# Kernel tuning notes

Hardware: AMD Instinct MI355X
Metric: run time of the kernel (lower is better)

## Reference

```python
import jax, jax.numpy as jnp
import numpy as np

EPS = 1.1920929e-07  # torch.finfo(torch.float32).eps
R = 2
K = 2 * R - 1  # 3x3 directional kernels

# kornia normalized sobel kernels (divided by sum of |k| = 8)
_SOBEL_X = np.array([[-1.0, 0.0, 1.0], [-2.0, 0.0, 2.0], [-1.0, 0.0, 1.0]], np.float32) / 8.0
_SOBEL_Y = _SOBEL_X.T.copy()


def _conv2d_same(x, k2d, pad_mode):
    """Depthwise 'same' cross-correlation of x:[B,C,H,W] with a single [kh,kw] kernel."""
    B, C, H, W = x.shape
    kh, kw = k2d.shape
    ph, pw = kh // 2, kw // 2
    xp = jnp.pad(x, ((0, 0), (0, 0), (ph, ph), (pw, pw)), mode=pad_mode)
    xr = xp.reshape(B * C, 1, H + 2 * ph, W + 2 * pw)
    kr = jnp.asarray(k2d, x.dtype)[None, None]  # [1,1,kh,kw]
    y = jax.lax.conv_general_dilated(
        xr, kr, window_strides=(1, 1), padding='VALID',
        dimension_numbers=('NCHW', 'OIHW', 'NCHW'))
    return y.reshape(B, C, H, W)


def _spatial_gradient(x):
    # kornia SpatialGradient(mode='sobel', normalized=True) with replicate padding
    gx = _conv2d_same(x, _SOBEL_X, 'edge')
    gy = _conv2d_same(x, _SOBEL_Y, 'edge')
    return gx, gy


def _edge_theta(true_labels):
    gx, gy = _spatial_gradient(true_labels)
    gxx, _ = _spatial_gradient(gx)       # second_grad_x[:, :, 0]
    gxy, gyy = _spatial_gradient(gy)     # second_grad_y[:, :, 0], [:, :, 1]
    theta = jnp.fmod(
        jnp.arctan(gyy * jnp.sign(-gxy + EPS) / (gxx + EPS)),
        np.float32(np.pi))
    return theta


def _directional_kernels():
    vert = np.zeros((K, K), np.float32); vert[:, R - 1] = 1.0   # ones column
    horiz = np.zeros((K, K), np.float32); horiz[R - 1, :] = 1.0  # ones row
    lead = np.eye(K, dtype=np.float32)
    cnt = np.fliplr(np.eye(K, dtype=np.float32)).copy()
    return horiz, vert, lead, cnt


def setup_inputs() -> dict:
    key = jax.random.key(0)
    k1, k2 = jax.random.split(key)
    true_labels = jax.random.uniform(k1, (8, 2, 1024, 1024), dtype=jnp.float32)
    pred_labels = jax.random.normal(k2, (8, 2, 1024, 1024), dtype=jnp.float32)
    return {"true_labels": true_labels, "pred_labels": pred_labels}


def reference(true_labels, pred_labels):
    theta = _edge_theta(true_labels)
    # quantize edge direction into 5 bins
    thresh_theta = jnp.fmod(jnp.round(theta * (5.0 / np.float32(np.pi))) + 5.0, 5.0)
    exp_preds = jnp.exp(pred_labels)

    horiz_k, vert_k, lead_k, cnt_k = _directional_kernels()
    # kornia filter2D default: reflect padding, no normalization
    horiz_f = _conv2d_same(exp_preds, horiz_k, 'reflect')
    vert_f = _conv2d_same(exp_preds, vert_k, 'reflect')
    lead_f = _conv2d_same(exp_preds, lead_k, 'reflect')
    cnt_f = _conv2d_same(exp_preds, cnt_k, 'reflect')

    horiz_nms = (thresh_theta == 0).astype(exp_preds.dtype) * (exp_preds / (horiz_f + EPS))
    vert_nms = (thresh_theta == 2).astype(exp_preds.dtype) * (exp_preds / (vert_f + EPS))
    lead_nms = (thresh_theta == 3).astype(exp_preds.dtype) * (exp_preds / (lead_f + EPS))
    cnt_nms = (thresh_theta == 1).astype(exp_preds.dtype) * (exp_preds / (cnt_f + EPS))

    # cat along new dim then total sum == sum of the four partial sums
    nms_loss = horiz_nms.sum() + vert_nms.sum() + lead_nms.sum() + cnt_nms.sum()
    return nms_loss
```

## Files before the change

### kernel.cpp

```cpp
#include <hip/hip_runtime.h>

#define HHI 1024
#define WWI 1024
#define NI  16
#define EPSF  1.1920929e-07f
#define EPS64 7.62939453125e-06f
#define T1 0.3249196962329063f
#define T2 1.3763819204711735f

#define GX  16
#define GYB 8
#define FRB 4
#define NB_INT (GX * GYB * NI)
#define NB_FRM (FRB * GYB * NI)
#define NB_TOT (NB_INT + NB_FRM)
#define NFRAME 8176

__device__ __forceinline__ int clampi(int v, int hi) { return v < 0 ? 0 : (v > hi ? hi : v); }
__device__ __forceinline__ int refli(int v, int n)  { return v < 0 ? -v : (v >= n ? 2*n-2-v : v); }
__device__ __forceinline__ float frcp(float x) { return __builtin_amdgcn_rcpf(x); }

template <bool USE_WS>
__global__ __launch_bounds__(256, 6) void nms_main(
    const float* __restrict__ tru, const float* __restrict__ prd,
    float* __restrict__ partial)
{
    __shared__ float sred[4];
    const int tid  = threadIdx.x;
    const int lane = tid & 63;
    const int wave = tid >> 6;
    const int z = blockIdx.z;
    const float* timg = tru + (size_t)z * (HHI * WWI);
    const float* pimg = prd + (size_t)z * (HHI * WWI);
    float term = 0.f;

    if (blockIdx.x < GX) {
        const int x  = blockIdx.x * 64 + lane;
        const int Y0 = blockIdx.y * 128 + wave * 32;
        const int ci0 = clampi(x - 2, WWI - 1);
        const int ci1 = clampi(x - 1, WWI - 1);
        const int ci2 = x;
        const int ci3 = clampi(x + 1, WWI - 1);
        const int ci4 = clampi(x + 2, WWI - 1);
        const bool mx = (x >= 2) & (x <= WWI - 3);
        float H1[5], H2[5], H3[5];
        #pragma unroll 1
        for (int ch = 0; ch < 8; ++ch) {
            #pragma unroll
            for (int pos = 0; pos < 5; ++pos) {
                const int i = ch * 5 + pos;
                if (i < 36) {
                    const int s  = Y0 - 2 + i;
                    const int gy = clampi(s, HHI - 1);
                    const float* trow = timg + (size_t)gy * WWI;
                    float t0 = trow[ci0], t1 = trow[ci1], t2 = trow[ci2],
                          t3 = trow[ci3], t4 = trow[ci4];
                    float s04 = t0 + t4, s13 = t1 + t3;
                    H1[pos] = s04 - 2.f * t2;
                    H2[pos] = s04 + 4.f * s13 + 6.f * t2;
                    H3[pos] = (t4 - t0) + 2.f * (t3 - t1);
                    if (i >= 4) {
                        const int y = s - 2;
                        if (y >= 2 && y <= HHI - 3) {
                            const int q0 = (pos + 1) % 5, q1 = (pos + 2) % 5,
                                      q2 = (pos + 3) % 5, q3 = (pos + 4) % 5, q4 = pos;
                            float gxx = (H1[q0] + H1[q4]) + 4.f * (H1[q1] + H1[q3]) + 6.f * H1[q2];
                            float gyy = (H2[q0] + H2[q4]) - 2.f * H2[q2];
                            float gxy = (H3[q4] - H3[q0]) + 2.f * (H3[q3] - H3[q1]);
                            float sarg = EPS64 - gxy;
                            float num = (sarg > 0.f) ? gyy : ((sarg < 0.f) ? -gyy : 0.f);
                            float v = num * frcp(gxx + EPS64);
                            bool c2v = (v > T2);
                            bool c1v = (v > T1) & !c2v;
                            bool c0v = (v >= -T1) & (v <= T1);
                            bool c3v = (v < -T2);
                            bool have = c2v | c1v | c0v | c3v;
                            int dr  = c0v ? 0 : 1;
                            int co1 = c2v ? ci2 : (c1v ? ci3 : ci1);
                            int co2 = c2v ? ci2 : (c1v ? ci1 : ci3);
                            float ec = __expf(pimg[(size_t)y * WWI + ci2]);
                            float d1 = __expf(pimg[(size_t)(y - dr) * WWI + co1]);
                            float d2 = __expf(pimg[(size_t)(y + dr) * WWI + co2]);
                            float val = ec * frcp(d1 + ec + d2 + EPSF);
                            term += (have & mx) ? val : 0.f;
                        }
                    }
                }
            }
        }
    } else {
        const int fid = (blockIdx.x - GX) * GYB + blockIdx.y;
        const int p = fid * 256 + tid;
        const bool valid = p < NFRAME;
        int y, x;
        if (p < 2048)      { y = p >> 10;                x = p & 1023; }
        else if (p < 4096) { y = 1022 + ((p - 2048) >> 10); x = p & 1023; }
        else { int q = p - 4096; y = 2 + (q >> 2); int xi = q & 3; x = (xi < 2) ? xi : 1020 + xi; }
        if (!valid) { y = 2; x = 0; }

        int R1[3], C1[3], R2[3][3], C2[3][3];
        #pragma unroll
        for (int a = 0; a < 3; ++a) { R1[a] = clampi(y + a - 1, HHI - 1); C1[a] = clampi(x + a - 1, WWI - 1); }
        #pragma unroll
        for (int a = 0; a < 3; ++a)
            #pragma unroll
            for (int e = 0; e < 3; ++e) {
                R2[a][e] = clampi(R1[a] + e - 1, HHI - 1);
                C2[a][e] = clampi(C1[a] + e - 1, WWI - 1);
            }
        const int hx[3] = {-1, 0, 1}, vx[3] = {1, 2, 1};
        const int hy[3] = {1, 2, 1},  vy[3] = {-1, 0, 1};
        float gxu[3][3], gyu[3][3];
        #pragma unroll
        for (int a = 0; a < 3; ++a)
            #pragma unroll
            for (int b = 0; b < 3; ++b) {
                float sx = 0.f, sy = 0.f;
                #pragma unroll
                for (int e = 0; e < 3; ++e)
                    #pragma unroll
                    for (int f = 0; f < 3; ++f) {
                        const int wx = hx[f] * vx[e], wy = hy[f] * vy[e];
                        if (wx | wy) {
                            float tv = timg[(size_t)R2[a][e] * WWI + C2[b][f]];
                            if (wx) sx += (float)wx * tv;
                            if (wy) sy += (float)wy * tv;
                        }
                    }
                gxu[a][b] = sx; gyu[a][b] = sy;
            }
        float gxx = 0.f, gxy = 0.f, gyy = 0.f;
        #pragma unroll
        for (int a = 0; a < 3; ++a)
            #pragma unroll
            for (int b = 0; b < 3; ++b) {
                const int w1 = hx[b] * vx[a], w2 = hy[b] * vy[a];
                if (w1) { gxx += (float)w1 * gxu[a][b]; gxy += (float)w1 * gyu[a][b]; }
                if (w2) { gyy += (float)w2 * gyu[a][b]; }
            }
        float sarg = EPS64 - gxy;
        float num = (sarg > 0.f) ? gyy : ((sarg < 0.f) ? -gyy : 0.f);
        float v = num * frcp(gxx + EPS64);
        bool c2v = (v > T2);
        bool c1v = (v > T1) & !c2v;
        bool c0v = (v >= -T1) & (v <= T1);
        bool c3v = (v < -T2);
        bool have = c2v | c1v | c0v | c3v;
        int r1 = c0v ? y : refli(y - 1, HHI);
        int r2 = c0v ? y : refli(y + 1, HHI);
        int xm = refli(x - 1, WWI), xp = refli(x + 1, WWI);
        int co1 = c2v ? x : (c1v ? xp : xm);
        int co2 = c2v ? x : (c1v ? xm : xp);
        float ec = __expf(pimg[(size_t)y * WWI + x]);
        float d1 = __expf(pimg[(size_t)r1 * WWI + co1]);
        float d2 = __expf(pimg[(size_t)r2 * WWI + co2]);
        float val = ec * frcp(d1 + ec + d2 + EPSF);
        term += (have & valid) ? val : 0.f;
    }

    for (int off = 32; off; off >>= 1) term += __shfl_down(term, off, 64);
    if (lane == 0) sred[wave] = term;
    __syncthreads();
    if (tid == 0) {
        float b = sred[0] + sred[1] + sred[2] + sred[3];
        if (USE_WS) {
            const int slot = (blockIdx.x < GX)
                ? ((z * GYB + blockIdx.y) * GX + blockIdx.x)
                : (NB_INT + z * 32 + ((blockIdx.x - GX) * GYB + blockIdx.y));
            partial[slot] = b;
        } else {
            atomicAdd(partial, b);
        }
    }
}

__global__ __launch_bounds__(1024) void reduce_kernel(
    const float* __restrict__ partial, float* __restrict__ out)
{
    __shared__ float s_red[16];
    float s = 0.f;
    for (int i = threadIdx.x; i < NB_TOT; i += 1024) s += partial[i];
    for (int off = 32; off; off >>= 1) s += __shfl_down(s, off, 64);
    if ((threadIdx.x & 63) == 0) s_red[threadIdx.x >> 6] = s;
    __syncthreads();
    if (threadIdx.x == 0) {
        float b = 0.f;
        #pragma unroll
        for (int i = 0; i < 16; ++i) b += s_red[i];
        out[0] = b;
    }
}

extern "C" void kernel_launch(void* const* d_in, const int* in_sizes, int n_in,
                              void* d_out, int out_size, void* d_ws, size_t ws_size,
                              hipStream_t stream) {
    const float* tru = (const float*)d_in[0];
    const float* prd = (const float*)d_in[1];
    float* out = (float*)d_out;
    dim3 grid(GX + FRB, GYB, NI);
    dim3 block(256, 1, 1);
    if (ws_size >= (size_t)NB_TOT * sizeof(float)) {
        float* ws = (float*)d_ws;
        hipLaunchKernelGGL(nms_main<true>, grid, block, 0, stream, tru, prd, ws);
        hipLaunchKernelGGL(reduce_kernel, dim3(1), dim3(1024), 0, stream, ws, out);
    } else {
        hipMemsetAsync(out, 0, sizeof(float), stream);
        hipLaunchKernelGGL(nms_main<false>, grid, block, 0, stream, tru, prd, out);
    }
}
```

Before: 69.44 us.

## Process four columns per thread with float4 loads and register-reused exp rows

Each thread now handles four adjacent columns using vectorized float4/float2 loads for both the label and prediction rows, and the exp of each prediction row is computed once into a rolling register window. The neighbour terms are selected from these registers instead of being gathered and recomputed with exp per pixel. The border-frame pixels are folded into the same blocks, handled by half of each wave after the interior loop, instead of needing separate frame blocks. This removes redundant exp calls and scattered global loads but raises register pressure, so the occupancy hint drops from 6 to 4 and there are fewer blocks.

```diff
diff --git a/kernel.cpp b/kernel.cpp
--- a/kernel.cpp
+++ b/kernel.cpp
@@ -3,25 +3,98 @@
 #define HHI 1024
 #define WWI 1024
 #define NI  16
+#define HWSZ (HHI * WWI)
 #define EPSF  1.1920929e-07f
 #define EPS64 7.62939453125e-06f
 #define T1 0.3249196962329063f
 #define T2 1.3763819204711735f
 
-#define GX  16
-#define GYB 8
-#define FRB 4
-#define NB_INT (GX * GYB * NI)
-#define NB_FRM (FRB * GYB * NI)
-#define NB_TOT (NB_INT + NB_FRM)
-#define NFRAME 8176
+#define SW 256
+#define RW 16
+#define GX  (WWI / SW)
+#define GYB (HHI / (RW * 4))
+#define NB  (GX * GYB * NI)
+#define FR_IMG 8176
+#define FR_TOT (FR_IMG * NI)
 
 __device__ __forceinline__ int clampi(int v, int hi) { return v < 0 ? 0 : (v > hi ? hi : v); }
 __device__ __forceinline__ int refli(int v, int n)  { return v < 0 ? -v : (v >= n ? 2*n-2-v : v); }
 __device__ __forceinline__ float frcp(float x) { return __builtin_amdgcn_rcpf(x); }
 
+#define STAGE(POS, IDX, DOPRED, DOOUT) do {                                           \
+    const int i_ = (IDX);                                                             \
+    {                                                                                 \
+        const int gy_ = clampi(Y0 - 2 + i_, HHI - 1);                                 \
+        const float* trow_ = timg + (size_t)gy_ * WWI;                                \
+        const float4 cq_ = *(const float4*)(trow_ + x0);                              \
+        const float2 lo_ = *(const float2*)(trow_ + cm2);                             \
+        const float2 hi_ = *(const float2*)(trow_ + cp4);                             \
+        float wv_[8];                                                                 \
+        wv_[0] = xokl ? lo_.x : cq_.x;                                                \
+        wv_[1] = xokl ? lo_.y : cq_.x;                                                \
+        wv_[2] = cq_.x; wv_[3] = cq_.y; wv_[4] = cq_.z; wv_[5] = cq_.w;               \
+        wv_[6] = xokr ? hi_.x : cq_.w;                                                \
+        wv_[7] = xokr ? hi_.y : cq_.w;                                                \
+        _Pragma("unroll")                                                             \
+        for (int k = 0; k < 4; ++k) {                                                 \
+            float s04 = wv_[k] + wv_[k+4];                                            \
+            float s13 = wv_[k+1] + wv_[k+3];                                          \
+            H1[POS][k] = s04 - 2.f * wv_[k+2];                                        \
+            H2[POS][k] = s04 + 4.f * s13 + 6.f * wv_[k+2];                            \
+            H3[POS][k] = (wv_[k+4] - wv_[k]) + 2.f * (wv_[k+3] - wv_[k+1]);           \
+        }                                                                             \
+    }                                                                                 \
+    if (DOPRED) {                                                                     \
+        const int gp_ = refli(Y0 + i_ - 3, HHI);                                      \
+        const float* prow_ = pimg + (size_t)gp_ * WWI;                                \
+        const float4 pq_ = *(const float4*)(prow_ + x0);                              \
+        const float pl_ = prow_[cm1];                                                 \
+        const float pr_ = prow_[cp4s];                                                \
+        Ec[POS][0] = __expf(pq_.x); Ec[POS][1] = __expf(pq_.y);                       \
+        Ec[POS][2] = __expf(pq_.z); Ec[POS][3] = __expf(pq_.w);                       \
+        El[POS] = __expf(xokl ? pl_ : pq_.y);           \
+        Er[POS] = __expf(xokr ? pr_ : pq_.z);             \
+    }                                                                                 \
+    if (DOOUT) {                                                                      \
+        const int y_ = Y0 + i_ - 4;                                                   \
+        const bool my_ = (y_ >= 2) & (y_ <= HHI - 3);                                 \
+        const int q0=(POS+1)%5, q1=(POS+2)%5, q2=(POS+3)%5, q3=(POS+4)%5, q4=POS;     \
+        const int e0=(POS+3)%5, e1=(POS+4)%5, e2=POS;                                 \
+        _Pragma("unroll")                                                             \
+        for (int k = 0; k < 4; ++k) {                                                 \
+            float gxx = (H1[q0][k]+H1[q4][k]) + 4.f*(H1[q1][k]+H1[q3][k]) + 6.f*H1[q2][k]; \
+            float gyy = (H2[q0][k]+H2[q4][k]) - 2.f*H2[q2][k];                        \
+            float gxy = (H3[q4][k]-H3[q0][k]) + 2.f*(H3[q3][k]-H3[q1][k]);            \
+            float sarg = EPS64 - gxy;                                                 \
+            float num = (sarg > 0.f) ? gyy : ((sarg < 0.f) ? -gyy : 0.f);             \
+            float v = num * frcp(gxx + EPS64);                                        \
+            bool c2v = (v > T2);                                                      \
+            bool c1v = (v > T1) & !c2v;                                               \
+            bool c0v = (v >= -T1) & (v <= T1);                                        \
+            bool c3v = (v < -T2);                                                     \
+            bool have = c2v | c1v | c0v | c3v;                       \
+            float r0m = (k==0) ? El[e0] : Ec[e0][(k>0)?k-1:0];                        \
+            float r0c = Ec[e0][k];                                                    \
+            float r0p = (k==3) ? Er[e0] : Ec[e0][(k<3)?k+1:3];                        \
+            float r1m = (k==0) ? El[e1] : Ec[e1][(k>0)?k-1:0];                        \
+            float r1c = Ec[e1][k];                                                    \
+            float r1p = (k==3) ? Er[e1] : Ec[e1][(k<3)?k+1:3];                        \
+            float r2m = (k==0) ? El[e2] : Ec[e2][(k>0)?k-1:0];                        \
+            float r2c = Ec[e2][k];                                                    \
+            float r2p = (k==3) ? Er[e2] : Ec[e2][(k<3)?k+1:3];                        \
+            float d1 = c0v ? r1m : (c2v ? r0c : (c1v ? r0p : r0m));                   \
+            float d2 = c0v ? r1p : (c2v ? r2c : (c1v ? r2m : r2p));                   \
+            float ec = r1c;                                                           \
+            float val = ec * frcp(d1 + ec + d2 + EPSF);                               \
+            const int x_ = x0 + k;                                                    \
+            bool ok = have & my_ & (x_ >= 2) & (x_ <= WWI - 3);                       \
+            term += ok ? val : 0.f;                                                   \
+        }                                                                             \
+    }                                                                                 \
+} while (0)
+
 template <bool USE_WS>
-__global__ __launch_bounds__(256, 6) void nms_main(
+__global__ __launch_bounds__(256, 4) void nms_main(
     const float* __restrict__ tru, const float* __restrict__ prd,
     float* __restrict__ partial)
 {
@@ -30,73 +103,51 @@
     const int lane = tid & 63;
     const int wave = tid >> 6;
     const int z = blockIdx.z;
-    const float* timg = tru + (size_t)z * (HHI * WWI);
-    const float* pimg = prd + (size_t)z * (HHI * WWI);
+    const float* timg = tru + (size_t)z * HWSZ;
+    const float* pimg = prd + (size_t)z * HWSZ;
     float term = 0.f;
 
-    if (blockIdx.x < GX) {
-        const int x  = blockIdx.x * 64 + lane;
-        const int Y0 = blockIdx.y * 128 + wave * 32;
-        const int ci0 = clampi(x - 2, WWI - 1);
-        const int ci1 = clampi(x - 1, WWI - 1);
-        const int ci2 = x;
-        const int ci3 = clampi(x + 1, WWI - 1);
-        const int ci4 = clampi(x + 2, WWI - 1);
-        const bool mx = (x >= 2) & (x <= WWI - 3);
-        float H1[5], H2[5], H3[5];
-        #pragma unroll 1
-        for (int ch = 0; ch < 8; ++ch) {
-            #pragma unroll
-            for (int pos = 0; pos < 5; ++pos) {
-                const int i = ch * 5 + pos;
-                if (i < 36) {
-                    const int s  = Y0 - 2 + i;
-                    const int gy = clampi(s, HHI - 1);
-                    const float* trow = timg + (size_t)gy * WWI;
-                    float t0 = trow[ci0], t1 = trow[ci1], t2 = trow[ci2],
-                          t3 = trow[ci3], t4 = trow[ci4];
-                    float s04 = t0 + t4, s13 = t1 + t3;
-                    H1[pos] = s04 - 2.f * t2;
-                    H2[pos] = s04 + 4.f * s13 + 6.f * t2;
-                    H3[pos] = (t4 - t0) + 2.f * (t3 - t1);
-                    if (i >= 4) {
-                        const int y = s - 2;
-                        if (y >= 2 && y <= HHI - 3) {
-                            const int q0 = (pos + 1) % 5, q1 = (pos + 2) % 5,
-                                      q2 = (pos + 3) % 5, q3 = (pos + 4) % 5, q4 = pos;
-                            float gxx = (H1[q0] + H1[q4]) + 4.f * (H1[q1] + H1[q3]) + 6.f * H1[q2];
-                            float gyy = (H2[q0] + H2[q4]) - 2.f * H2[q2];
-                            float gxy = (H3[q4] - H3[q0]) + 2.f * (H3[q3] - H3[q1]);
-                            float sarg = EPS64 - gxy;
-                            float num = (sarg > 0.f) ? gyy : ((sarg < 0.f) ? -gyy : 0.f);
-                            float v = num * frcp(gxx + EPS64);
-                            bool c2v = (v > T2);
-                            bool c1v = (v > T1) & !c2v;
-                            bool c0v = (v >= -T1) & (v <= T1);
-                            bool c3v = (v < -T2);
-                            bool have = c2v | c1v | c0v | c3v;
-                            int dr  = c0v ? 0 : 1;
-                            int co1 = c2v ? ci2 : (c1v ? ci3 : ci1);
-                            int co2 = c2v ? ci2 : (c1v ? ci1 : ci3);
-                            float ec = __expf(pimg[(size_t)y * WWI + ci2]);
-                            float d1 = __expf(pimg[(size_t)(y - dr) * WWI + co1]);
-                            float d2 = __expf(pimg[(size_t)(y + dr) * WWI + co2]);
-                            float val = ec * frcp(d1 + ec + d2 + EPSF);
-                            term += (have & mx) ? val : 0.f;
-                        }
-                    }
-                }
-            }
-        }
-    } else {
-        const int fid = (blockIdx.x - GX) * GYB + blockIdx.y;
-        const int p = fid * 256 + tid;
-        const bool valid = p < NFRAME;
+    const int X0 = blockIdx.x * SW;
+    const int x0 = X0 + lane * 4;
+    const int Y0 = blockIdx.y * (RW * 4) + wave * RW;
+    const bool xokl = (x0 >= 2);
+    const bool xokr = (x0 + 4 <= WWI - 1);
+    const int cm2  = xokl ? x0 - 2 : 0;
+    const int cp4  = xokr ? x0 + 4 : WWI - 2;
+    const int cm1  = xokl ? x0 - 1 : 0;
+    const int cp4s = xokr ? x0 + 4 : WWI - 1;
+
+    float H1[5][4], H2[5][4], H3[5][4];
+    float Ec[5][4], El[5], Er[5];
+
+    STAGE(0, 0, 0, 0);
+    STAGE(1, 1, 0, 0);
+    STAGE(2, 2, 1, 0);
+    STAGE(3, 3, 1, 0);
+    STAGE(4, 4, 1, 1);
+    #pragma unroll 1
+    for (int g = 1; g < 4; ++g) {
+        const int ib = g * 5;
+        STAGE(0, ib + 0, 1, 1);
+        STAGE(1, ib + 1, 1, 1);
+        STAGE(2, ib + 2, 1, 1);
+        STAGE(3, ib + 3, 1, 1);
+        STAGE(4, ib + 4, 1, 1);
+    }
+
+    {
+        const int wid = (((z * gridDim.y) + blockIdx.y) * gridDim.x + blockIdx.x) * 4 + wave;
+        int fp = wid * 32 + lane;
+        const bool valid = (lane < 32) && (fp < FR_TOT);
+        if (fp >= FR_TOT) fp = FR_TOT - 1;
+        const int fz = fp / FR_IMG;
+        const int p  = fp - fz * FR_IMG;
+        const float* ftim = tru + (size_t)fz * HWSZ;
+        const float* fpim = prd + (size_t)fz * HWSZ;
         int y, x;
-        if (p < 2048)      { y = p >> 10;                x = p & 1023; }
+        if (p < 2048)      { y = p >> 10;                   x = p & 1023; }
         else if (p < 4096) { y = 1022 + ((p - 2048) >> 10); x = p & 1023; }
         else { int q = p - 4096; y = 2 + (q >> 2); int xi = q & 3; x = (xi < 2) ? xi : 1020 + xi; }
-        if (!valid) { y = 2; x = 0; }
 
         int R1[3], C1[3], R2[3][3], C2[3][3];
         #pragma unroll
@@ -122,7 +173,7 @@
                     for (int f = 0; f < 3; ++f) {
                         const int wx = hx[f] * vx[e], wy = hy[f] * vy[e];
                         if (wx | wy) {
-                            float tv = timg[(size_t)R2[a][e] * WWI + C2[b][f]];
+                            float tv = ftim[(size_t)R2[a][e] * WWI + C2[b][f]];
                             if (wx) sx += (float)wx * tv;
                             if (wy) sy += (float)wy * tv;
                         }
@@ -151,11 +202,11 @@
         int xm = refli(x - 1, WWI), xp = refli(x + 1, WWI);
         int co1 = c2v ? x : (c1v ? xp : xm);
         int co2 = c2v ? x : (c1v ? xm : xp);
-        float ec = __expf(pimg[(size_t)y * WWI + x]);
-        float d1 = __expf(pimg[(size_t)r1 * WWI + co1]);
-        float d2 = __expf(pimg[(size_t)r2 * WWI + co2]);
-        float val = ec * frcp(d1 + ec + d2 + EPSF);
-        term += (have & valid) ? val : 0.f;
+        float ecf = __expf(fpim[(size_t)y * WWI + x]);
+        float d1f = __expf(fpim[(size_t)r1 * WWI + co1]);
+        float d2f = __expf(fpim[(size_t)r2 * WWI + co2]);
+        float fval = ecf * frcp(d1f + ecf + d2f + EPSF);
+        term += (have & valid) ? fval : 0.f;
     }
 
     for (int off = 32; off; off >>= 1) term += __shfl_down(term, off, 64);
@@ -164,10 +215,7 @@
     if (tid == 0) {
         float b = sred[0] + sred[1] + sred[2] + sred[3];
         if (USE_WS) {
-            const int slot = (blockIdx.x < GX)
-                ? ((z * GYB + blockIdx.y) * GX + blockIdx.x)
-                : (NB_INT + z * 32 + ((blockIdx.x - GX) * GYB + blockIdx.y));
-            partial[slot] = b;
+            partial[((size_t)z * gridDim.y + blockIdx.y) * gridDim.x + blockIdx.x] = b;
         } else {
             atomicAdd(partial, b);
         }
@@ -179,7 +227,7 @@
 {
     __shared__ float s_red[16];
     float s = 0.f;
-    for (int i = threadIdx.x; i < NB_TOT; i += 1024) s += partial[i];
+    for (int i = threadIdx.x; i < NB; i += 1024) s += partial[i];
     for (int off = 32; off; off >>= 1) s += __shfl_down(s, off, 64);
     if ((threadIdx.x & 63) == 0) s_red[threadIdx.x >> 6] = s;
     __syncthreads();
@@ -197,9 +245,9 @@
     const float* tru = (const float*)d_in[0];
     const float* prd = (const float*)d_in[1];
     float* out = (float*)d_out;
-    dim3 grid(GX + FRB, GYB, NI);
+    dim3 grid(GX, GYB, NI);
     dim3 block(256, 1, 1);
-    if (ws_size >= (size_t)NB_TOT * sizeof(float)) {
+    if (ws_size >= (size_t)NB * sizeof(float)) {
         float* ws = (float*)d_ws;
         hipLaunchKernelGGL(nms_main<true>, grid, block, 0, stream, tru, prd, ws);
         hipLaunchKernelGGL(reduce_kernel, dim3(1), dim3(1024), 0, stream, ws, out);
```

Result: slower. 84.89 us (+22.3%).

## Stage exp(pred) rows in per-wave LDS ring to avoid redundant gathers

Applied to the files above, without the earlier changes.

The interior path now computes exp(pred) once per pixel per row and stores it in a per-wave 4-row shared-memory ring with halo columns. Neighbour lookups for the directional NMS come from LDS instead of three scattered global loads and three exps per pixel. The row loop is fully unrolled through a macro so the ring indices are compile-time constants. This adds LDS traffic and more code size in exchange for fewer global gathers and transcendental ops. No barrier is placed between the ring writes and reads; this relies on each ring being private to one wave.

```diff
diff --git a/kernel.cpp b/kernel.cpp
--- a/kernel.cpp
+++ b/kernel.cpp
@@ -3,6 +3,7 @@
 #define HHI 1024
 #define WWI 1024
 #define NI  16
+#define HWSZ (HHI * WWI)
 #define EPSF  1.1920929e-07f
 #define EPS64 7.62939453125e-06f
 #define T1 0.3249196962329063f
@@ -12,88 +13,105 @@
 #define GYB 8
 #define FRB 4
 #define NB_INT (GX * GYB * NI)
-#define NB_FRM (FRB * GYB * NI)
-#define NB_TOT (NB_INT + NB_FRM)
+#define NB_TOT ((GX + FRB) * GYB * NI)
 #define NFRAME 8176
 
 __device__ __forceinline__ int clampi(int v, int hi) { return v < 0 ? 0 : (v > hi ? hi : v); }
 __device__ __forceinline__ int refli(int v, int n)  { return v < 0 ? -v : (v >= n ? 2*n-2-v : v); }
 __device__ __forceinline__ float frcp(float x) { return __builtin_amdgcn_rcpf(x); }
+
+#define STAGE(IDX, DOPRED, DOOUT) do {                                        \
+    {                                                                         \
+        const int gy_ = clampi(Y0 - 2 + (IDX), HHI - 1);                      \
+        const float* trow_ = timg + (size_t)gy_ * WWI;                        \
+        float t0 = trow_[ci0], t1 = trow_[ci1], t2 = trow_[ci2],              \
+              t3 = trow_[ci3], t4 = trow_[ci4];                               \
+        float s04 = t0 + t4, s13 = t1 + t3;                                   \
+        H1[(IDX)%5] = s04 - 2.f * t2;                      \
+        H2[(IDX)%5] = s04 + 4.f * s13 + 6.f * t2;          \
+        H3[(IDX)%5] = (t4 - t0) + 2.f * (t3 - t1);         \
+    }                                                                         \
+    if (DOPRED) {                                                             \
+        const float* prow_ = pimg + (size_t)refli(Y0 + (IDX) - 3, HHI) * WWI; \
+        ecP = ecC; ecC = __expf(prow_[ci2]);                                  \
+        wring[((IDX)&3)*66 + lane + 1] = ecC;                                 \
+        if (lane == 0)  wring[((IDX)&3)*66]      = __expf(prow_[pcL]);        \
+        if (lane == 63) wring[((IDX)&3)*66 + 65] = __expf(prow_[pcR]);        \
+    }                                                                         \
+    if (DOOUT) {                                                              \
+        const int y_ = Y0 + (IDX) - 4;                                        \
+        const int q0=((IDX)+1)%5, q1=((IDX)+2)%5, q2=((IDX)+3)%5,             \
+                  q3=((IDX)+4)%5, q4=(IDX)%5;                                 \
+        float gxx = (H1[q0]+H1[q4]) + 4.f*(H1[q1]+H1[q3]) + 6.f*H1[q2];       \
+        float gyy = (H2[q0]+H2[q4]) - 2.f*H2[q2];                             \
+        float gxy = (H3[q4]-H3[q0]) + 2.f*(H3[q3]-H3[q1]);                    \
+        float sarg = EPS64 - gxy;                                             \
+        float num = (sarg > 0.f) ? gyy : ((sarg < 0.f) ? -gyy : 0.f);         \
+        float v = num * frcp(gxx + EPS64);                                    \
+        bool c2v = (v > T2);                                                  \
+        bool c1v = (v > T1) & !c2v;                                           \
+        bool c0v = (v >= -T1) & (v <= T1);                                    \
+        bool c3v = (v < -T2);                                                 \
+        bool have = c2v | c1v | c0v | c3v;                   \
+        const int sT = (((IDX)+2)&3)*66;                       \
+        const int sM = (((IDX)+3)&3)*66;                       \
+        const int sB = ((IDX)&3)*66;                                          \
+        int dc1 = c0v ? -1 : (c2v ? 0 : (c1v ? 1 : -1));                      \
+        float d1 = wring[(c0v ? sM : sT) + lane + 1 + dc1];                   \
+        float d2 = wring[(c0v ? sM : sB) + lane + 1 - dc1];                   \
+        float val = ecP * frcp(d1 + ecP + d2 + EPSF);                         \
+        bool ok = have & mx & (y_ >= 2) & (y_ <= HHI - 3);                    \
+        term += ok ? val : 0.f;                                               \
+    }                                                                         \
+} while (0)
 
 template <bool USE_WS>
 __global__ __launch_bounds__(256, 6) void nms_main(
     const float* __restrict__ tru, const float* __restrict__ prd,
     float* __restrict__ partial)
 {
+    __shared__ float ring[4][4 * 66];
     __shared__ float sred[4];
     const int tid  = threadIdx.x;
     const int lane = tid & 63;
     const int wave = tid >> 6;
     const int z = blockIdx.z;
-    const float* timg = tru + (size_t)z * (HHI * WWI);
-    const float* pimg = prd + (size_t)z * (HHI * WWI);
+    const float* timg = tru + (size_t)z * HWSZ;
+    const float* pimg = prd + (size_t)z * HWSZ;
     float term = 0.f;
 
     if (blockIdx.x < GX) {
-        const int x  = blockIdx.x * 64 + lane;
+        const int X0 = blockIdx.x * 64;
+        const int x  = X0 + lane;
         const int Y0 = blockIdx.y * 128 + wave * 32;
+        const bool mx = (x >= 2) & (x <= WWI - 3);
         const int ci0 = clampi(x - 2, WWI - 1);
         const int ci1 = clampi(x - 1, WWI - 1);
         const int ci2 = x;
         const int ci3 = clampi(x + 1, WWI - 1);
         const int ci4 = clampi(x + 2, WWI - 1);
-        const bool mx = (x >= 2) & (x <= WWI - 3);
+        const int pcL = refli(X0 - 1, WWI);
+        const int pcR = refli(X0 + 64, WWI);
+        float* wring = &ring[wave][0];
+
         float H1[5], H2[5], H3[5];
-        #pragma unroll 1
-        for (int ch = 0; ch < 8; ++ch) {
-            #pragma unroll
-            for (int pos = 0; pos < 5; ++pos) {
-                const int i = ch * 5 + pos;
-                if (i < 36) {
-                    const int s  = Y0 - 2 + i;
-                    const int gy = clampi(s, HHI - 1);
-                    const float* trow = timg + (size_t)gy * WWI;
-                    float t0 = trow[ci0], t1 = trow[ci1], t2 = trow[ci2],
-                          t3 = trow[ci3], t4 = trow[ci4];
-                    float s04 = t0 + t4, s13 = t1 + t3;
-                    H1[pos] = s04 - 2.f * t2;
-                    H2[pos] = s04 + 4.f * s13 + 6.f * t2;
-                    H3[pos] = (t4 - t0) + 2.f * (t3 - t1);
-                    if (i >= 4) {
-                        const int y = s - 2;
-                        if (y >= 2 && y <= HHI - 3) {
-                            const int q0 = (pos + 1) % 5, q1 = (pos + 2) % 5,
-                                      q2 = (pos + 3) % 5, q3 = (pos + 4) % 5, q4 = pos;
-                            float gxx = (H1[q0] + H1[q4]) + 4.f * (H1[q1] + H1[q3]) + 6.f * H1[q2];
-                            float gyy = (H2[q0] + H2[q4]) - 2.f * H2[q2];
-                            float gxy = (H3[q4] - H3[q0]) + 2.f * (H3[q3] - H3[q1]);
-                            float sarg = EPS64 - gxy;
-                            float num = (sarg > 0.f) ? gyy : ((sarg < 0.f) ? -gyy : 0.f);
-                            float v = num * frcp(gxx + EPS64);
-                            bool c2v = (v > T2);
-                            bool c1v = (v > T1) & !c2v;
-                            bool c0v = (v >= -T1) & (v <= T1);
-                            bool c3v = (v < -T2);
-                            bool have = c2v | c1v | c0v | c3v;
-                            int dr  = c0v ? 0 : 1;
-                            int co1 = c2v ? ci2 : (c1v ? ci3 : ci1);
-                            int co2 = c2v ? ci2 : (c1v ? ci1 : ci3);
-                            float ec = __expf(pimg[(size_t)y * WWI + ci2]);
-                            float d1 = __expf(pimg[(size_t)(y - dr) * WWI + co1]);
-                            float d2 = __expf(pimg[(size_t)(y + dr) * WWI + co2]);
-                            float val = ec * frcp(d1 + ec + d2 + EPSF);
-                            term += (have & mx) ? val : 0.f;
-                        }
-                    }
-                }
-            }
-        }
+        float ecP = 0.f, ecC = 0.f;
+
+        STAGE(0, 0, 0);  STAGE(1, 0, 0);  STAGE(2, 1, 0);  STAGE(3, 1, 0);
+        STAGE(4, 1, 1);  STAGE(5, 1, 1);  STAGE(6, 1, 1);  STAGE(7, 1, 1);
+        STAGE(8, 1, 1);  STAGE(9, 1, 1);  STAGE(10, 1, 1); STAGE(11, 1, 1);
+        STAGE(12, 1, 1); STAGE(13, 1, 1); STAGE(14, 1, 1); STAGE(15, 1, 1);
+        STAGE(16, 1, 1); STAGE(17, 1, 1); STAGE(18, 1, 1); STAGE(19, 1, 1);
+        STAGE(20, 1, 1); STAGE(21, 1, 1); STAGE(22, 1, 1); STAGE(23, 1, 1);
+        STAGE(24, 1, 1); STAGE(25, 1, 1); STAGE(26, 1, 1); STAGE(27, 1, 1);
+        STAGE(28, 1, 1); STAGE(29, 1, 1); STAGE(30, 1, 1); STAGE(31, 1, 1);
+        STAGE(32, 1, 1); STAGE(33, 1, 1); STAGE(34, 1, 1); STAGE(35, 1, 1);
     } else {
         const int fid = (blockIdx.x - GX) * GYB + blockIdx.y;
         const int p = fid * 256 + tid;
         const bool valid = p < NFRAME;
         int y, x;
-        if (p < 2048)      { y = p >> 10;                x = p & 1023; }
+        if (p < 2048)      { y = p >> 10;                   x = p & 1023; }
         else if (p < 4096) { y = 1022 + ((p - 2048) >> 10); x = p & 1023; }
         else { int q = p - 4096; y = 2 + (q >> 2); int xi = q & 3; x = (xi < 2) ? xi : 1020 + xi; }
         if (!valid) { y = 2; x = 0; }
@@ -151,11 +169,11 @@
         int xm = refli(x - 1, WWI), xp = refli(x + 1, WWI);
         int co1 = c2v ? x : (c1v ? xp : xm);
         int co2 = c2v ? x : (c1v ? xm : xp);
-        float ec = __expf(pimg[(size_t)y * WWI + x]);
-        float d1 = __expf(pimg[(size_t)r1 * WWI + co1]);
-        float d2 = __expf(pimg[(size_t)r2 * WWI + co2]);
-        float val = ec * frcp(d1 + ec + d2 + EPSF);
-        term += (have & valid) ? val : 0.f;
+        float ecf = __expf(pimg[(size_t)y * WWI + x]);
+        float d1f = __expf(pimg[(size_t)r1 * WWI + co1]);
+        float d2f = __expf(pimg[(size_t)r2 * WWI + co2]);
+        float fval = ecf * frcp(d1f + ecf + d2f + EPSF);
+        term += (have & valid) ? fval : 0.f;
     }
 
     for (int off = 32; off; off >>= 1) term += __shfl_down(term, off, 64);
```

New measurement: 206.4 us. +197.2%, slower.
